# Optimization experiments

Measured on AMD Instinct MI355X. Metric: run time of the kernel, lower is better.

Reference implementation:

```python
import jax, jax.numpy as jnp
import numpy as np

NH = 8       # num attention heads (hardcoded in module)
NL = 6       # n_layers
EPS = 1e-5   # LayerNorm eps (torch default)


def pos_enc(dim, length):
    # faithful to module's positional_encoding: even cols sin, odd cols cos,
    # with angle = pos / 10000^(2i/dim) where i indexes ALL columns via arange(0,2*dim,2)/dim
    pos = jnp.arange(length, dtype=jnp.float32)[:, None]
    div = 1.0 / (10000.0 ** (jnp.arange(0, 2 * dim, 2, dtype=jnp.float32) / dim))
    ang = pos * div[None, :]  # [length, dim]
    cols = jnp.arange(dim)
    return jnp.where(cols % 2 == 0, jnp.sin(ang), jnp.cos(ang))


def layernorm(x):
    m = x.mean(-1, keepdims=True)
    v = x.var(-1, keepdims=True)  # biased, matches torch LayerNorm
    return (x - m) / jnp.sqrt(v + EPS)


def setup_inputs() -> dict:
    key = jax.random.key(0)
    ks = jax.random.split(key, 8)
    S, H = 2048, 1024
    D = H // NH
    sc = 1.0 / np.sqrt(H)  # ~ torch Linear init scale
    return {
        "inputs": jax.random.normal(ks[0], (S, H), jnp.float32),
        "Wq": jax.random.normal(ks[1], (NH, H, D), jnp.float32) * sc,
        "bq": jnp.zeros((NH, D), jnp.float32),
        "Wk": jax.random.normal(ks[2], (NH, H, D), jnp.float32) * sc,
        "bk": jnp.zeros((NH, D), jnp.float32),
        "Wv": jax.random.normal(ks[3], (NH, H, D), jnp.float32) * sc,
        "bv": jnp.zeros((NH, D), jnp.float32),
        "W1": jax.random.normal(ks[4], (H, H), jnp.float32) * sc,
        "b1": jnp.zeros((H,), jnp.float32),
        "W2": jax.random.normal(ks[5], (H, H), jnp.float32) * sc,
        "b2": jnp.zeros((H,), jnp.float32),
    }


def reference(inputs, Wq, bq, Wk, bk, Wv, bv, W1, b1, W2, b2):
    S, H = inputs.shape
    scale = jnp.sqrt(jnp.float32(H))  # module scales by sqrt(hidden), not sqrt(head_dim)
    x = inputs + pos_enc(H, S)        # [S, H]
    kv = x  # dropout in eval mode = identity; k_v_input fixed to layer-0 input (faithful)
    # K/V are identical every layer (shared weights + fixed kv input)
    K = jnp.einsum('sh,nhd->nsd', kv, Wk) + bk[:, None, :]  # [NH, S, D]
    V = jnp.einsum('sh,nhd->nsd', kv, Wv) + bv[:, None, :]
    t_in = x
    for _ in range(NL):
        Q = jnp.einsum('sh,nhd->nsd', t_in, Wq) + bq[:, None, :]
        A = jax.nn.softmax(jnp.einsum('nsd,ntd->nst', Q, K) / scale, axis=-1)
        ctx = jnp.einsum('nst,ntd->nsd', A, V)        # [NH, S, D]
        cat = ctx.transpose(1, 0, 2).reshape(S, H)    # concat heads on feature dim
        mh = layernorm(t_in + cat)
        ff = jax.nn.relu(mh @ W1 + b1) @ W2 + b2
        t_in = layernorm(mh + ff)
    return t_in
```

## Files before the change

### kernel.cpp

```cpp
#include <hip/hip_runtime.h>

#define S_LEN 2048
#define H_DIM 1024
#define NHEAD 8
#define D_HEAD 128
#define KSPLIT 2
#define KV_PER (S_LEN / KSPLIT)

typedef __bf16 bf16x8 __attribute__((ext_vector_type(8)));
typedef float floatx4 __attribute__((ext_vector_type(4)));

__device__ __forceinline__ float b2f(unsigned short u) {
    union { unsigned int i; float f; } v;
    v.i = ((unsigned int)u) << 16;
    return v.f;
}
__device__ __forceinline__ unsigned short f2b(float f) {
    union { float f; unsigned int i; } v;
    v.f = f;
    return (unsigned short)((v.i + 0x7fffu + ((v.i >> 16) & 1u)) >> 16);
}

__device__ __forceinline__ void dma16(void* lds, const void* g) {
    __builtin_amdgcn_global_load_lds(
        (const __attribute__((address_space(1))) void*)g,
        (__attribute__((address_space(3))) void*)lds, 16, 0, 0);
}

__global__ __launch_bounds__(256) void posenc_kernel(
    const float* __restrict__ in, float* __restrict__ xf,
    unsigned short* __restrict__ xb)
{
    int g = blockIdx.x * 256 + threadIdx.x;
    int s = g >> 10;
    int h = g & 1023;
    float dv = powf(10000.0f, -(float)h * (1.0f / 512.0f));
    float ang = (float)s * dv;
    float pe = (h & 1) ? cosf(ang) : sinf(ang);
    float x = in[g] + pe;
    xf[g] = x;
    xb[g] = f2b(x);
}

__global__ __launch_bounds__(256) void transpose_all(
    const float* __restrict__ Wq, const float* __restrict__ Wk,
    const float* __restrict__ Wv, const float* __restrict__ W1,
    const float* __restrict__ W2,
    unsigned short* __restrict__ WqT, unsigned short* __restrict__ WkT,
    unsigned short* __restrict__ WvT, unsigned short* __restrict__ W1T,
    unsigned short* __restrict__ W2T)
{
    __shared__ unsigned short tile[32][33];
    const int z = blockIdx.z;
    const float* ih;
    unsigned short* oh;
    int ldin;
    if (z < 8)       { ih = Wq + (size_t)z * 131072;        oh = WqT + (size_t)z * 131072;        ldin = 128; }
    else if (z < 16) { ih = Wk + (size_t)(z - 8) * 131072;  oh = WkT + (size_t)(z - 8) * 131072;  ldin = 128; }
    else if (z < 24) { ih = Wv + (size_t)(z - 16) * 131072; oh = WvT + (size_t)(z - 16) * 131072; ldin = 128; }
    else if (z < 32) { ih = W1 + (size_t)(z - 24) * 128;    oh = W1T + (size_t)(z - 24) * 131072; ldin = 1024; }
    else             { ih = W2 + (size_t)(z - 32) * 128;    oh = W2T + (size_t)(z - 32) * 131072; ldin = 1024; }
    const int r0 = blockIdx.y * 32, c0 = blockIdx.x * 32;
    const int tx = threadIdx.x, ty = threadIdx.y;
    for (int i = ty; i < 32; i += 8)
        tile[i][tx] = f2b(ih[(size_t)(r0 + i) * ldin + c0 + tx]);
    __syncthreads();
    for (int i = ty; i < 32; i += 8)
        oh[(size_t)(c0 + i) * 1024 + r0 + tx] = tile[tx][i];
}

template <int MODE, bool RELU>
__device__ __forceinline__ void gemm128_core(
    unsigned short* sA, unsigned short* sB,
    const unsigned short* A, const unsigned short* Bt,
    const float* bias, float* Cf, unsigned short* Cb, int ldt, int i0, int j0)
{
    const int K = H_DIM;
    const int tid = threadIdx.x;
    const int wave = tid >> 6, lane = tid & 63;
    const int quad = lane >> 4, l16 = lane & 15;
    const int wm = (wave >> 1) * 64, wn = (wave & 1) * 64;

    const int srow = lane >> 3;
    const int schunk = (lane & 7) ^ srow;
    const unsigned short* Ap = A + (size_t)(i0 + wave * 8 + srow) * K + schunk * 8;
    const unsigned short* Bp = Bt + (size_t)(j0 + wave * 8 + srow) * K + schunk * 8;

    floatx4 z4 = {0.f, 0.f, 0.f, 0.f};
    floatx4 acc[4][4];
#pragma unroll
    for (int i = 0; i < 4; i++)
#pragma unroll
        for (int j = 0; j < 4; j++) acc[i][j] = z4;

#pragma unroll
    for (int it = 0; it < 4; it++) {
        const int lb = (wave * 8 + it * 32) * 64;
        dma16(sA + lb, Ap + (size_t)(it * 32) * K);
        dma16(sB + lb, Bp + (size_t)(it * 32) * K);
    }
    __syncthreads();

    int buf = 0;
    for (int k0 = 0; k0 < K; k0 += 64) {
        if (k0 + 64 < K) {
            unsigned short* nA = sA + (buf ^ 1) * 8192;
            unsigned short* nB = sB + (buf ^ 1) * 8192;
#pragma unroll
            for (int it = 0; it < 4; it++) {
                const int lb = (wave * 8 + it * 32) * 64;
                dma16(nA + lb, Ap + (size_t)(it * 32) * K + k0 + 64);
                dma16(nB + lb, Bp + (size_t)(it * 32) * K + k0 + 64);
            }
        }
        const unsigned short* cA = sA + buf * 8192;
        const unsigned short* cB = sB + buf * 8192;
#pragma unroll
        for (int kh = 0; kh < 2; kh++) {
            bf16x8 af[4], bfr[4];
#pragma unroll
            for (int mi = 0; mi < 4; mi++) {
                int row = wm + mi * 16 + l16;
                int p = (kh * 4 + quad) ^ (l16 & 7);
                af[mi] = *(const bf16x8*)(cA + row * 64 + p * 8);
            }
#pragma unroll
            for (int ni = 0; ni < 4; ni++) {
                int row = wn + ni * 16 + l16;
                int p = (kh * 4 + quad) ^ (l16 & 7);
                bfr[ni] = *(const bf16x8*)(cB + row * 64 + p * 8);
            }
#pragma unroll
            for (int mi = 0; mi < 4; mi++)
#pragma unroll
                for (int ni = 0; ni < 4; ni++)
                    acc[mi][ni] = __builtin_amdgcn_mfma_f32_16x16x32_bf16(
                        af[mi], bfr[ni], acc[mi][ni], 0, 0, 0);
        }
        __syncthreads();
        buf ^= 1;
    }

#pragma unroll
    for (int mi = 0; mi < 4; mi++) {
#pragma unroll
        for (int ni = 0; ni < 4; ni++) {
            const int col = j0 + wn + ni * 16 + l16;
            const float bval = bias[col];
#pragma unroll
            for (int r = 0; r < 4; r++) {
                const int row_o = i0 + wm + mi * 16 + quad * 4 + r;
                float v = acc[mi][ni][r] + bval;
                if (RELU) v = fmaxf(v, 0.0f);
                if (MODE == 0) Cb[(size_t)row_o * H_DIM + col] = f2b(v);
                else if (MODE == 1) Cb[(size_t)col * ldt + row_o] = f2b(v);
                else Cf[(size_t)row_o * H_DIM + col] = v;
            }
        }
    }
}

template <int MODE, bool RELU>
__global__ __launch_bounds__(256, 2) void gemm128(
    const unsigned short* __restrict__ A, const unsigned short* __restrict__ Bt,
    const float* __restrict__ bias, float* __restrict__ Cf,
    unsigned short* __restrict__ Cb, int ldt)
{
    extern __shared__ __align__(16) unsigned short gsm[];
    gemm128_core<MODE, RELU>(gsm, gsm + 16384, A, Bt, bias, Cf, Cb, ldt,
                             blockIdx.y * 128, blockIdx.x * 128);
}

__global__ __launch_bounds__(256, 2) void gemm_kv(
    const unsigned short* __restrict__ A,
    const unsigned short* __restrict__ WkT, const unsigned short* __restrict__ WvT,
    const float* __restrict__ bk, const float* __restrict__ bv,
    unsigned short* __restrict__ Kb, unsigned short* __restrict__ Vtb)
{
    extern __shared__ __align__(16) unsigned short gsm[];
    if (blockIdx.z == 0)
        gemm128_core<0, false>(gsm, gsm + 16384, A, WkT, bk, nullptr, Kb, 0,
                               blockIdx.y * 128, blockIdx.x * 128);
    else
        gemm128_core<1, false>(gsm, gsm + 16384, A, WvT, bv, nullptr, Vtb, S_LEN,
                               blockIdx.y * 128, blockIdx.x * 128);
}

__global__ __launch_bounds__(256, 2) void flash_attn(
    const unsigned short* __restrict__ Qg, const unsigned short* __restrict__ Kg,
    const unsigned short* __restrict__ Vt, unsigned short* __restrict__ Op,
    float* __restrict__ Lp)
{
    extern __shared__ __align__(16) unsigned short smem[];
    unsigned short* sK0 = smem;
    unsigned short* sV0 = smem + 16384;
    unsigned short* sP = smem + 32768;

    const int tid = threadIdx.x;
    const int wave = tid >> 6, lane = tid & 63;
    const int quad = lane >> 4, l16 = lane & 15;
    const int head = blockIdx.y;
    const int q0 = blockIdx.x * 64;
    const int split = blockIdx.z;
    const int h0 = head * D_HEAD;

    bf16x8 aq[4];
    const int qrow = q0 + wave * 16 + l16;
#pragma unroll
    for (int ks = 0; ks < 4; ks++)
        aq[ks] = *(const bf16x8*)(Qg + (size_t)qrow * H_DIM + h0 + ks * 32 + quad * 8);

    unsigned short* myP = sP + wave * (16 * 72);

    const int k_r = wave * 4 + (lane >> 4);
    const int k_c = (lane & 15) ^ (k_r & 15);
    const int v_r = wave * 8 + (lane >> 3);
    const int v_c = (lane & 7) ^ (v_r & 7);

    const unsigned short* Kbase = Kg + h0;
    const unsigned short* Vbase = Vt + (size_t)h0 * S_LEN;
    const int kt0 = split * KV_PER;

    floatx4 z4 = {0.f, 0.f, 0.f, 0.f};
    floatx4 o[8];
#pragma unroll
    for (int i = 0; i < 8; i++) o[i] = z4;
    float l_r[4] = {0.f, 0.f, 0.f, 0.f};

#pragma unroll
    for (int it = 0; it < 4; it++) {
        dma16(sK0 + (wave * 4 + it * 16) * 128,
              Kbase + (size_t)(kt0 + k_r + it * 16) * H_DIM + k_c * 8);
        dma16(sV0 + (wave * 8 + it * 32) * 64,
              Vbase + (size_t)(v_r + it * 32) * S_LEN + kt0 + v_c * 8);
    }
    __syncthreads();

    int buf = 0;
    for (int it0 = 0; it0 < KV_PER; it0 += 64) {
        const int t0 = kt0 + it0;
        if (it0 + 64 < KV_PER) {
            const int nt = t0 + 64;
            unsigned short* nK = sK0 + (buf ^ 1) * 8192;
            unsigned short* nV = sV0 + (buf ^ 1) * 8192;
#pragma unroll
            for (int it = 0; it < 4; it++) {
                dma16(nK + (wave * 4 + it * 16) * 128,
                      Kbase + (size_t)(nt + k_r + it * 16) * H_DIM + k_c * 8);
                dma16(nV + (wave * 8 + it * 32) * 64,
                      Vbase + (size_t)(v_r + it * 32) * S_LEN + nt + v_c * 8);
            }
        }
        const unsigned short* cK = sK0 + buf * 8192;
        const unsigned short* cV = sV0 + buf * 8192;

        floatx4 sc[4];
#pragma unroll
        for (int ni = 0; ni < 4; ni++) {
            sc[ni] = z4;
#pragma unroll
            for (int ks = 0; ks < 4; ks++) {
                int p = (ks * 4 + quad) ^ l16;
                bf16x8 bk = *(const bf16x8*)(cK + (ni * 16 + l16) * 128 + p * 8);
                sc[ni] = __builtin_amdgcn_mfma_f32_16x16x32_bf16(aq[ks], bk, sc[ni], 0, 0, 0);
            }
        }

#pragma unroll
        for (int ni = 0; ni < 4; ni++)
#pragma unroll
            for (int r = 0; r < 4; r++) {
                float p = __expf(sc[ni][r] * 0.03125f);
                sc[ni][r] = p;
                l_r[r] += p;
            }

#pragma unroll
        for (int ni = 0; ni < 4; ni++)
#pragma unroll
            for (int r = 0; r < 4; r++) {
                int prow = quad * 4 + r;
                myP[prow * 72 + ((ni * 16 + l16) ^ ((prow & 8) << 1))] = f2b(sc[ni][r]);
            }
        bf16x8 ap[2];
#pragma unroll
        for (int ks = 0; ks < 2; ks++)
            ap[ks] = *(const bf16x8*)(myP + l16 * 72 + ((ks * 32 + quad * 8) ^ ((l16 & 8) << 1)));

#pragma unroll
        for (int ni = 0; ni < 8; ni++) {
#pragma unroll
            for (int ks = 0; ks < 2; ks++) {
                int p = (ks * 4 + quad) ^ (l16 & 7);
                bf16x8 bv = *(const bf16x8*)(cV + (ni * 16 + l16) * 64 + p * 8);
                o[ni] = __builtin_amdgcn_mfma_f32_16x16x32_bf16(ap[ks], bv, o[ni], 0, 0, 0);
            }
        }

        __syncthreads();
        buf ^= 1;
    }

#pragma unroll
    for (int r = 0; r < 4; r++)
#pragma unroll
        for (int off = 1; off < 16; off <<= 1)
            l_r[r] += __shfl_xor(l_r[r], off, 64);

#pragma unroll
    for (int r = 0; r < 4; r++) {
        float inv = 1.0f / l_r[r];
        int row = q0 + wave * 16 + quad * 4 + r;
#pragma unroll
        for (int ni = 0; ni < 8; ni++)
            Op[((size_t)split * S_LEN + row) * H_DIM + h0 + ni * 16 + l16] =
                f2b(o[ni][r] * inv);
        if (l16 == 0)
            Lp[(split * NHEAD + head) * S_LEN + row] = l_r[r];
    }
}

__global__ __launch_bounds__(256) void merge_add_layernorm(
    const float* __restrict__ t, const unsigned short* __restrict__ Op,
    const float* __restrict__ Lp,
    float* __restrict__ of, unsigned short* __restrict__ ob)
{
    __shared__ float red[8];
    const int row = blockIdx.x, tid = threadIdx.x;
    const int head = tid >> 5;
    const size_t base = (size_t)row * H_DIM + tid * 4;

    float l_s[KSPLIT];
    ushort4 os[KSPLIT];
#pragma unroll
    for (int sp = 0; sp < KSPLIT; sp++) {
        os[sp] = *(const ushort4*)(Op + ((size_t)sp * S_LEN + row) * H_DIM + tid * 4);
        l_s[sp] = Lp[(sp * NHEAD + head) * S_LEN + row];
    }
    float W = 0.f, a0 = 0.f, a1 = 0.f, a2 = 0.f, a3 = 0.f;
#pragma unroll
    for (int sp = 0; sp < KSPLIT; sp++) {
        float w = l_s[sp];
        W += w;
        a0 += w * b2f(os[sp].x);
        a1 += w * b2f(os[sp].y);
        a2 += w * b2f(os[sp].z);
        a3 += w * b2f(os[sp].w);
    }
    float inv = 1.0f / W;
    float4 x = *(const float4*)(t + base);
    float v0 = x.x + a0 * inv, v1 = x.y + a1 * inv;
    float v2 = x.z + a2 * inv, v3 = x.w + a3 * inv;

    float s = v0 + v1 + v2 + v3;
    float q = v0 * v0 + v1 * v1 + v2 * v2 + v3 * v3;
#pragma unroll
    for (int off = 32; off >= 1; off >>= 1) {
        s += __shfl_xor(s, off, 64);
        q += __shfl_xor(q, off, 64);
    }
    if ((tid & 63) == 0) { red[tid >> 6] = s; red[4 + (tid >> 6)] = q; }
    __syncthreads();
    s = red[0] + red[1] + red[2] + red[3];
    q = red[4] + red[5] + red[6] + red[7];
    const float mean = s * (1.0f / (float)H_DIM);
    const float var = q * (1.0f / (float)H_DIM) - mean * mean;
    const float rstd = rsqrtf(var + 1e-5f);
    float o0 = (v0 - mean) * rstd, o1 = (v1 - mean) * rstd;
    float o2 = (v2 - mean) * rstd, o3 = (v3 - mean) * rstd;
    *(float4*)(of + base) = make_float4(o0, o1, o2, o3);
    *(ushort4*)(ob + base) = make_ushort4(f2b(o0), f2b(o1), f2b(o2), f2b(o3));
}

__global__ __launch_bounds__(256) void add_layernorm(
    const float* __restrict__ a, const float* __restrict__ b,
    float* __restrict__ of, unsigned short* __restrict__ ob)
{
    __shared__ float red[8];
    const int row = blockIdx.x, tid = threadIdx.x;
    const size_t base = (size_t)row * H_DIM + tid * 4;
    float4 x = *(const float4*)(a + base);
    float4 y = *(const float4*)(b + base);
    float v0 = x.x + y.x, v1 = x.y + y.y, v2 = x.z + y.z, v3 = x.w + y.w;
    float s = v0 + v1 + v2 + v3;
    float q = v0 * v0 + v1 * v1 + v2 * v2 + v3 * v3;
#pragma unroll
    for (int off = 32; off >= 1; off >>= 1) {
        s += __shfl_xor(s, off, 64);
        q += __shfl_xor(q, off, 64);
    }
    if ((tid & 63) == 0) { red[tid >> 6] = s; red[4 + (tid >> 6)] = q; }
    __syncthreads();
    s = red[0] + red[1] + red[2] + red[3];
    q = red[4] + red[5] + red[6] + red[7];
    const float mean = s * (1.0f / (float)H_DIM);
    const float var = q * (1.0f / (float)H_DIM) - mean * mean;
    const float rstd = rsqrtf(var + 1e-5f);
    float o0 = (v0 - mean) * rstd, o1 = (v1 - mean) * rstd;
    float o2 = (v2 - mean) * rstd, o3 = (v3 - mean) * rstd;
    *(float4*)(of + base) = make_float4(o0, o1, o2, o3);
    *(ushort4*)(ob + base) = make_ushort4(f2b(o0), f2b(o1), f2b(o2), f2b(o3));
}

extern "C" void kernel_launch(void* const* d_in, const int* in_sizes, int n_in,
                              void* d_out, int out_size, void* d_ws, size_t ws_size,
                              hipStream_t stream)
{
    (void)in_sizes; (void)n_in; (void)out_size; (void)ws_size;
    const float* in = (const float*)d_in[0];
    const float* Wq = (const float*)d_in[1];
    const float* bq = (const float*)d_in[2];
    const float* Wk = (const float*)d_in[3];
    const float* bk = (const float*)d_in[4];
    const float* Wv = (const float*)d_in[5];
    const float* bv = (const float*)d_in[6];
    const float* W1 = (const float*)d_in[7];
    const float* b1 = (const float*)d_in[8];
    const float* W2 = (const float*)d_in[9];
    const float* b2 = (const float*)d_in[10];

    char* ws = (char*)d_ws;
    const size_t MB = 1024 * 1024;
    float* t_f32 = (float*)(ws + 0 * MB);
    float* cf_f32 = (float*)(ws + 8 * MB);
    unsigned short* t_b = (unsigned short*)(ws + 16 * MB);
    unsigned short* K_b = (unsigned short*)(ws + 20 * MB);
    unsigned short* Vt_b = (unsigned short*)(ws + 24 * MB);
    unsigned short* Q_b = (unsigned short*)(ws + 28 * MB);
    unsigned short* WqT = (unsigned short*)(ws + 32 * MB);
    unsigned short* WkT = (unsigned short*)(ws + 34 * MB);
    unsigned short* WvT = (unsigned short*)(ws + 36 * MB);
    unsigned short* W1T = (unsigned short*)(ws + 38 * MB);
    unsigned short* W2T = (unsigned short*)(ws + 40 * MB);
    unsigned short* Op = (unsigned short*)(ws + 42 * MB);
    float* Lp = (float*)(ws + 58 * MB);

    (void)hipFuncSetAttribute(reinterpret_cast<const void*>(&flash_attn),
                              hipFuncAttributeMaxDynamicSharedMemorySize, 74752);
    (void)hipFuncSetAttribute(reinterpret_cast<const void*>(&gemm128<0, false>),
                              hipFuncAttributeMaxDynamicSharedMemorySize, 65536);
    (void)hipFuncSetAttribute(reinterpret_cast<const void*>(&gemm128<0, true>),
                              hipFuncAttributeMaxDynamicSharedMemorySize, 65536);
    (void)hipFuncSetAttribute(reinterpret_cast<const void*>(&gemm128<2, false>),
                              hipFuncAttributeMaxDynamicSharedMemorySize, 65536);
    (void)hipFuncSetAttribute(reinterpret_cast<const void*>(&gemm_kv),
                              hipFuncAttributeMaxDynamicSharedMemorySize, 65536);

    transpose_all<<<dim3(4, 32, 40), dim3(32, 8), 0, stream>>>(
        Wq, Wk, Wv, W1, W2, WqT, WkT, WvT, W1T, W2T);

    posenc_kernel<<<(S_LEN * H_DIM) / 256, 256, 0, stream>>>(in, t_f32, t_b);

    dim3 gg(H_DIM / 128, S_LEN / 128);
    gemm_kv<<<dim3(8, 16, 2), 256, 65536, stream>>>(t_b, WkT, WvT, bk, bv, K_b, Vt_b);

    for (int layer = 0; layer < 6; layer++) {
        gemm128<0, false><<<gg, 256, 65536, stream>>>(t_b, WqT, bq, nullptr, Q_b, 0);
        flash_attn<<<dim3(S_LEN / 64, NHEAD, KSPLIT), 256, 74752, stream>>>(Q_b, K_b, Vt_b, Op, Lp);
        merge_add_layernorm<<<S_LEN, 256, 0, stream>>>(t_f32, Op, Lp, t_f32, t_b);
        gemm128<0, true><<<gg, 256, 65536, stream>>>(t_b, W1T, b1, nullptr, Q_b, 0);
        gemm128<2, false><<<gg, 256, 65536, stream>>>(Q_b, W2T, b2, cf_f32, nullptr, 0);
        float* of = (layer == 5) ? (float*)d_out : t_f32;
        add_layernorm<<<S_LEN, 256, 0, stream>>>(t_f32, cf_f32, of, t_b);
    }
}
```

Measured before the change: 593.9 us.

## Fuse split-KV merge and residual layernorms into GEMM A-operand staging

Removes the separate merge_add_layernorm and per-layer add_layernorm kernels. Each GEMM block now computes row statistics for its 128 rows and normalizes the residual sum on the fly while staging the bf16 A tile. Blocks with j0==0 also write the fp32 normalized rows needed for the next residual. This saves launches and intermediate round trips, but each of the 8 column blocks recomputes the row statistics and the A-tile loads become synchronous register work. A separate change remaps block indices so that blocks sharing rows land on the same XCD for L2 reuse.

New measurement: 2.335 ms. 3.93x slower.

```diff
diff --git a/kernel.cpp b/kernel.cpp
--- a/kernel.cpp
+++ b/kernel.cpp
@@ -9,6 +9,7 @@
 
 typedef __bf16 bf16x8 __attribute__((ext_vector_type(8)));
 typedef float floatx4 __attribute__((ext_vector_type(4)));
+typedef unsigned short ushortx8 __attribute__((ext_vector_type(8)));
 
 __device__ __forceinline__ float b2f(unsigned short u) {
     union { unsigned int i; float f; } v;
@@ -25,6 +26,13 @@
     __builtin_amdgcn_global_load_lds(
         (const __attribute__((address_space(1))) void*)g,
         (__attribute__((address_space(3))) void*)lds, 16, 0, 0);
+}
+
+__device__ __forceinline__ void xcd_map(int& i0, int& j0) {
+    int id = blockIdx.x + (blockIdx.y << 3);
+    int xcd = id & 7, slot = id >> 3;
+    i0 = (xcd + ((slot >> 3) << 3)) * 128;
+    j0 = (slot & 7) * 128;
 }
 
 __global__ __launch_bounds__(256) void posenc_kernel(
@@ -69,22 +77,168 @@
         oh[(size_t)(c0 + i) * 1024 + r0 + tx] = tile[tx][i];
 }
 
-template <int MODE, bool RELU>
-__device__ __forceinline__ void gemm128_core(
-    unsigned short* sA, unsigned short* sB,
-    const unsigned short* A, const unsigned short* Bt,
-    const float* bias, float* Cf, unsigned short* Cb, int ldt, int i0, int j0)
-{
-    const int K = H_DIM;
+template <int FUSE>
+__device__ __forceinline__ void stageA_f(
+    unsigned short* dstA, int kn, int i0,
+    const float* in1, const float* in2,
+    const unsigned short* OpP, const float* sW,
+    const float* my_m, const float* my_r, int wave, int lane)
+{
+    const int srow = lane >> 3;
+    const int schunk = (lane & 7) ^ srow;
+    const int h = kn >> 7;
+#pragma unroll
+    for (int it = 0; it < 4; it++) {
+        const int rl = wave * 8 + srow + it * 32;
+        const size_t gb = (size_t)(i0 + rl) * H_DIM + kn + schunk * 8;
+        float v[8];
+        float4 a0 = *(const float4*)(in1 + gb);
+        float4 a1 = *(const float4*)(in1 + gb + 4);
+        if (FUSE == 1) {
+            float4 b0 = *(const float4*)(in2 + gb);
+            float4 b1 = *(const float4*)(in2 + gb + 4);
+            v[0] = a0.x + b0.x; v[1] = a0.y + b0.y; v[2] = a0.z + b0.z; v[3] = a0.w + b0.w;
+            v[4] = a1.x + b1.x; v[5] = a1.y + b1.y; v[6] = a1.z + b1.z; v[7] = a1.w + b1.w;
+        } else {
+            const unsigned short* o0 = OpP + gb;
+            const unsigned short* o1 = o0 + (size_t)S_LEN * H_DIM;
+            ushort4 u0 = *(const ushort4*)o0, u1 = *(const ushort4*)(o0 + 4);
+            ushort4 t0 = *(const ushort4*)o1, t1 = *(const ushort4*)(o1 + 4);
+            float w0 = sW[(rl * 8 + h) * 2], w1 = sW[(rl * 8 + h) * 2 + 1];
+            v[0] = a0.x + w0 * b2f(u0.x) + w1 * b2f(t0.x);
+            v[1] = a0.y + w0 * b2f(u0.y) + w1 * b2f(t0.y);
+            v[2] = a0.z + w0 * b2f(u0.z) + w1 * b2f(t0.z);
+            v[3] = a0.w + w0 * b2f(u0.w) + w1 * b2f(t0.w);
+            v[4] = a1.x + w0 * b2f(u1.x) + w1 * b2f(t1.x);
+            v[5] = a1.y + w0 * b2f(u1.y) + w1 * b2f(t1.y);
+            v[6] = a1.z + w0 * b2f(u1.z) + w1 * b2f(t1.z);
+            v[7] = a1.w + w0 * b2f(u1.w) + w1 * b2f(t1.w);
+        }
+        const float m = my_m[it], rs = my_r[it];
+        ushortx8 pk;
+#pragma unroll
+        for (int e = 0; e < 8; e++) pk[e] = f2b((v[e] - m) * rs);
+        *(ushortx8*)(dstA + rl * 64 + (lane & 7) * 8) = pk;
+    }
+}
+
+template <int MODE, bool RELU, int FUSE>
+__device__ __forceinline__ void gemm_core(
+    unsigned short* sA, unsigned short* sB, float* sStat, float* sW,
+    const unsigned short* Abf, const unsigned short* Bt, const float* bias,
+    float* Cf, unsigned short* Cb, int ldt,
+    const float* in1, const float* in2,
+    const unsigned short* OpP, const float* LpP, float* xout,
+    int i0, int j0)
+{
     const int tid = threadIdx.x;
     const int wave = tid >> 6, lane = tid & 63;
     const int quad = lane >> 4, l16 = lane & 15;
     const int wm = (wave >> 1) * 64, wn = (wave & 1) * 64;
-
     const int srow = lane >> 3;
     const int schunk = (lane & 7) ^ srow;
-    const unsigned short* Ap = A + (size_t)(i0 + wave * 8 + srow) * K + schunk * 8;
-    const unsigned short* Bp = Bt + (size_t)(j0 + wave * 8 + srow) * K + schunk * 8;
+
+    float my_m[4], my_r[4];
+
+    if (FUSE) {
+        if (FUSE == 2) {
+            for (int e = tid; e < 1024; e += 256) {
+                int r = e >> 3, h = e & 7;
+                float l0 = LpP[h * S_LEN + i0 + r];
+                float l1 = LpP[(NHEAD + h) * S_LEN + i0 + r];
+                float inv = 1.f / (l0 + l1);
+                sW[e * 2] = l0 * inv; sW[e * 2 + 1] = l1 * inv;
+            }
+            __syncthreads();
+        }
+        {
+            const int r = tid >> 1, hf = tid & 1;
+            const float* p1 = in1 + (size_t)(i0 + r) * H_DIM + hf * 512;
+            float s = 0.f, q = 0.f;
+            if (FUSE == 1) {
+                const float* p2 = in2 + (size_t)(i0 + r) * H_DIM + hf * 512;
+                for (int c = 0; c < 512; c += 4) {
+                    float4 a = *(const float4*)(p1 + c);
+                    float4 b = *(const float4*)(p2 + c);
+                    float v0 = a.x + b.x, v1 = a.y + b.y, v2 = a.z + b.z, v3 = a.w + b.w;
+                    s += v0 + v1 + v2 + v3;
+                    q += v0 * v0 + v1 * v1 + v2 * v2 + v3 * v3;
+                }
+            } else {
+                const unsigned short* o0 = OpP + (size_t)(i0 + r) * H_DIM + hf * 512;
+                const unsigned short* o1 = o0 + (size_t)S_LEN * H_DIM;
+                for (int h4 = 0; h4 < 4; h4++) {
+                    int h = hf * 4 + h4;
+                    float w0 = sW[(r * 8 + h) * 2], w1 = sW[(r * 8 + h) * 2 + 1];
+                    for (int c = h4 * 128; c < h4 * 128 + 128; c += 4) {
+                        float4 a = *(const float4*)(p1 + c);
+                        ushort4 u = *(const ushort4*)(o0 + c);
+                        ushort4 t = *(const ushort4*)(o1 + c);
+                        float v0 = a.x + w0 * b2f(u.x) + w1 * b2f(t.x);
+                        float v1 = a.y + w0 * b2f(u.y) + w1 * b2f(t.y);
+                        float v2 = a.z + w0 * b2f(u.z) + w1 * b2f(t.z);
+                        float v3 = a.w + w0 * b2f(u.w) + w1 * b2f(t.w);
+                        s += v0 + v1 + v2 + v3;
+                        q += v0 * v0 + v1 * v1 + v2 * v2 + v3 * v3;
+                    }
+                }
+            }
+            s += __shfl_xor(s, 1, 64);
+            q += __shfl_xor(q, 1, 64);
+            if (hf == 0) {
+                float mean = s * (1.f / 1024.f);
+                float var = q * (1.f / 1024.f) - mean * mean;
+                sStat[r * 2] = mean;
+                sStat[r * 2 + 1] = rsqrtf(var + 1e-5f);
+            }
+        }
+        __syncthreads();
+        if (xout != nullptr && j0 == 0) {
+            const int r = tid >> 1, hf = tid & 1;
+            const float mean = sStat[r * 2], rstd = sStat[r * 2 + 1];
+            float* po = xout + (size_t)(i0 + r) * H_DIM + hf * 512;
+            const float* p1 = in1 + (size_t)(i0 + r) * H_DIM + hf * 512;
+            if (FUSE == 1) {
+                const float* p2 = in2 + (size_t)(i0 + r) * H_DIM + hf * 512;
+                for (int c = 0; c < 512; c += 4) {
+                    float4 a = *(const float4*)(p1 + c);
+                    float4 b = *(const float4*)(p2 + c);
+                    float4 o;
+                    o.x = (a.x + b.x - mean) * rstd; o.y = (a.y + b.y - mean) * rstd;
+                    o.z = (a.z + b.z - mean) * rstd; o.w = (a.w + b.w - mean) * rstd;
+                    *(float4*)(po + c) = o;
+                }
+            } else {
+                const unsigned short* o0 = OpP + (size_t)(i0 + r) * H_DIM + hf * 512;
+                const unsigned short* o1 = o0 + (size_t)S_LEN * H_DIM;
+                for (int h4 = 0; h4 < 4; h4++) {
+                    int h = hf * 4 + h4;
+                    float w0 = sW[(r * 8 + h) * 2], w1 = sW[(r * 8 + h) * 2 + 1];
+                    for (int c = h4 * 128; c < h4 * 128 + 128; c += 4) {
+                        float4 a = *(const float4*)(p1 + c);
+                        ushort4 u = *(const ushort4*)(o0 + c);
+                        ushort4 t = *(const ushort4*)(o1 + c);
+                        float4 o;
+                        o.x = (a.x + w0 * b2f(u.x) + w1 * b2f(t.x) - mean) * rstd;
+                        o.y = (a.y + w0 * b2f(u.y) + w1 * b2f(t.y) - mean) * rstd;
+                        o.z = (a.z + w0 * b2f(u.z) + w1 * b2f(t.z) - mean) * rstd;
+                        o.w = (a.w + w0 * b2f(u.w) + w1 * b2f(t.w) - mean) * rstd;
+                        *(float4*)(po + c) = o;
+                    }
+                }
+            }
+        }
+#pragma unroll
+        for (int it = 0; it < 4; it++) {
+            int rl = wave * 8 + srow + it * 32;
+            my_m[it] = sStat[rl * 2];
+            my_r[it] = sStat[rl * 2 + 1];
+        }
+    }
+
+    const unsigned short* Ap = (FUSE == 0)
+        ? Abf + (size_t)(i0 + wave * 8 + srow) * H_DIM + schunk * 8 : nullptr;
+    const unsigned short* Bp = Bt + (size_t)(j0 + wave * 8 + srow) * H_DIM + schunk * 8;
 
     floatx4 z4 = {0.f, 0.f, 0.f, 0.f};
     floatx4 acc[4][4];
@@ -93,24 +247,34 @@
 #pragma unroll
         for (int j = 0; j < 4; j++) acc[i][j] = z4;
 
-#pragma unroll
-    for (int it = 0; it < 4; it++) {
-        const int lb = (wave * 8 + it * 32) * 64;
-        dma16(sA + lb, Ap + (size_t)(it * 32) * K);
-        dma16(sB + lb, Bp + (size_t)(it * 32) * K);
-    }
+    if (FUSE == 0) {
+#pragma unroll
+        for (int it = 0; it < 4; it++)
+            dma16(sA + (wave * 8 + it * 32) * 64, Ap + (size_t)(it * 32) * H_DIM);
+    } else {
+        stageA_f<FUSE>(sA, 0, i0, in1, in2, OpP, sW, my_m, my_r, wave, lane);
+    }
+#pragma unroll
+    for (int it = 0; it < 4; it++)
+        dma16(sB + (wave * 8 + it * 32) * 64, Bp + (size_t)(it * 32) * H_DIM);
     __syncthreads();
 
     int buf = 0;
-    for (int k0 = 0; k0 < K; k0 += 64) {
-        if (k0 + 64 < K) {
+    for (int k0 = 0; k0 < H_DIM; k0 += 64) {
+        if (k0 + 64 < H_DIM) {
             unsigned short* nA = sA + (buf ^ 1) * 8192;
             unsigned short* nB = sB + (buf ^ 1) * 8192;
 #pragma unroll
-            for (int it = 0; it < 4; it++) {
-                const int lb = (wave * 8 + it * 32) * 64;
-                dma16(nA + lb, Ap + (size_t)(it * 32) * K + k0 + 64);
-                dma16(nB + lb, Bp + (size_t)(it * 32) * K + k0 + 64);
+            for (int it = 0; it < 4; it++)
+                dma16(nB + (wave * 8 + it * 32) * 64,
+                      Bp + (size_t)(it * 32) * H_DIM + k0 + 64);
+            if (FUSE == 0) {
+#pragma unroll
+                for (int it = 0; it < 4; it++)
+                    dma16(nA + (wave * 8 + it * 32) * 64,
+                          Ap + (size_t)(it * 32) * H_DIM + k0 + 64);
+            } else {
+                stageA_f<FUSE>(nA, k0 + 64, i0, in1, in2, OpP, sW, my_m, my_r, wave, lane);
             }
         }
         const unsigned short* cA = sA + buf * 8192;
@@ -161,14 +325,42 @@
 }
 
 template <int MODE, bool RELU>
-__global__ __launch_bounds__(256, 2) void gemm128(
+__global__ __launch_bounds__(256, 2) void gemm_plain(
     const unsigned short* __restrict__ A, const unsigned short* __restrict__ Bt,
     const float* __restrict__ bias, float* __restrict__ Cf,
-    unsigned short* __restrict__ Cb, int ldt)
+    unsigned short* __restrict__ Cb)
 {
     extern __shared__ __align__(16) unsigned short gsm[];
-    gemm128_core<MODE, RELU>(gsm, gsm + 16384, A, Bt, bias, Cf, Cb, ldt,
-                             blockIdx.y * 128, blockIdx.x * 128);
+    int i0, j0; xcd_map(i0, j0);
+    gemm_core<MODE, RELU, 0>(gsm, gsm + 16384, nullptr, nullptr, A, Bt, bias,
+                             Cf, Cb, 0, nullptr, nullptr, nullptr, nullptr, nullptr,
+                             i0, j0);
+}
+
+__global__ __launch_bounds__(256, 2) void gemm_fuse_add(
+    const float* __restrict__ in1, const float* __restrict__ in2,
+    const unsigned short* __restrict__ Bt, const float* __restrict__ bias,
+    unsigned short* __restrict__ Cb, float* __restrict__ xout)
+{
+    extern __shared__ __align__(16) unsigned short gsm[];
+    int i0, j0; xcd_map(i0, j0);
+    gemm_core<0, false, 1>(gsm, gsm + 16384, (float*)(gsm + 32768), nullptr,
+                           nullptr, Bt, bias, nullptr, Cb, 0,
+                           in1, in2, nullptr, nullptr, xout, i0, j0);
+}
+
+__global__ __launch_bounds__(256, 2) void gemm_fuse_merge(
+    const float* __restrict__ x, const unsigned short* __restrict__ OpP,
+    const float* __restrict__ LpP,
+    const unsigned short* __restrict__ Bt, const float* __restrict__ bias,
+    unsigned short* __restrict__ Cb, float* __restrict__ mhout)
+{
+    extern __shared__ __align__(16) unsigned short gsm[];
+    int i0, j0; xcd_map(i0, j0);
+    float* sStat = (float*)(gsm + 32768);
+    gemm_core<0, true, 2>(gsm, gsm + 16384, sStat, sStat + 256,
+                          nullptr, Bt, bias, nullptr, Cb, 0,
+                          x, nullptr, OpP, LpP, mhout, i0, j0);
 }
 
 __global__ __launch_bounds__(256, 2) void gemm_kv(
@@ -178,12 +370,15 @@
     unsigned short* __restrict__ Kb, unsigned short* __restrict__ Vtb)
 {
     extern __shared__ __align__(16) unsigned short gsm[];
+    int i0, j0; xcd_map(i0, j0);
     if (blockIdx.z == 0)
-        gemm128_core<0, false>(gsm, gsm + 16384, A, WkT, bk, nullptr, Kb, 0,
-                               blockIdx.y * 128, blockIdx.x * 128);
+        gemm_core<0, false, 0>(gsm, gsm + 16384, nullptr, nullptr, A, WkT, bk,
+                               nullptr, Kb, 0, nullptr, nullptr, nullptr, nullptr,
+                               nullptr, i0, j0);
     else
-        gemm128_core<1, false>(gsm, gsm + 16384, A, WvT, bv, nullptr, Vtb, S_LEN,
-                               blockIdx.y * 128, blockIdx.x * 128);
+        gemm_core<1, false, 0>(gsm, gsm + 16384, nullptr, nullptr, A, WvT, bv,
+                               nullptr, Vtb, S_LEN, nullptr, nullptr, nullptr,
+                               nullptr, nullptr, i0, j0);
 }
 
 __global__ __launch_bounds__(256, 2) void flash_attn(
@@ -320,61 +515,9 @@
     }
 }
 
-__global__ __launch_bounds__(256) void merge_add_layernorm(
-    const float* __restrict__ t, const unsigned short* __restrict__ Op,
-    const float* __restrict__ Lp,
-    float* __restrict__ of, unsigned short* __restrict__ ob)
-{
-    __shared__ float red[8];
-    const int row = blockIdx.x, tid = threadIdx.x;
-    const int head = tid >> 5;
-    const size_t base = (size_t)row * H_DIM + tid * 4;
-
-    float l_s[KSPLIT];
-    ushort4 os[KSPLIT];
-#pragma unroll
-    for (int sp = 0; sp < KSPLIT; sp++) {
-        os[sp] = *(const ushort4*)(Op + ((size_t)sp * S_LEN + row) * H_DIM + tid * 4);
-        l_s[sp] = Lp[(sp * NHEAD + head) * S_LEN + row];
-    }
-    float W = 0.f, a0 = 0.f, a1 = 0.f, a2 = 0.f, a3 = 0.f;
-#pragma unroll
-    for (int sp = 0; sp < KSPLIT; sp++) {
-        float w = l_s[sp];
-        W += w;
-        a0 += w * b2f(os[sp].x);
-        a1 += w * b2f(os[sp].y);
-        a2 += w * b2f(os[sp].z);
-        a3 += w * b2f(os[sp].w);
-    }
-    float inv = 1.0f / W;
-    float4 x = *(const float4*)(t + base);
-    float v0 = x.x + a0 * inv, v1 = x.y + a1 * inv;
-    float v2 = x.z + a2 * inv, v3 = x.w + a3 * inv;
-
-    float s = v0 + v1 + v2 + v3;
-    float q = v0 * v0 + v1 * v1 + v2 * v2 + v3 * v3;
-#pragma unroll
-    for (int off = 32; off >= 1; off >>= 1) {
-        s += __shfl_xor(s, off, 64);
-        q += __shfl_xor(q, off, 64);
-    }
-    if ((tid & 63) == 0) { red[tid >> 6] = s; red[4 + (tid >> 6)] = q; }
-    __syncthreads();
-    s = red[0] + red[1] + red[2] + red[3];
-    q = red[4] + red[5] + red[6] + red[7];
-    const float mean = s * (1.0f / (float)H_DIM);
-    const float var = q * (1.0f / (float)H_DIM) - mean * mean;
-    const float rstd = rsqrtf(var + 1e-5f);
-    float o0 = (v0 - mean) * rstd, o1 = (v1 - mean) * rstd;
-    float o2 = (v2 - mean) * rstd, o3 = (v3 - mean) * rstd;
-    *(float4*)(of + base) = make_float4(o0, o1, o2, o3);
-    *(ushort4*)(ob + base) = make_ushort4(f2b(o0), f2b(o1), f2b(o2), f2b(o3));
-}
-
 __global__ __launch_bounds__(256) void add_layernorm(
     const float* __restrict__ a, const float* __restrict__ b,
-    float* __restrict__ of, unsigned short* __restrict__ ob)
+    float* __restrict__ of)
 {
     __shared__ float red[8];
     const int row = blockIdx.x, tid = threadIdx.x;
@@ -396,10 +539,8 @@
     const float mean = s * (1.0f / (float)H_DIM);
     const float var = q * (1.0f / (float)H_DIM) - mean * mean;
     const float rstd = rsqrtf(var + 1e-5f);
-    float o0 = (v0 - mean) * rstd, o1 = (v1 - mean) * rstd;
-    float o2 = (v2 - mean) * rstd, o3 = (v3 - mean) * rstd;
-    *(float4*)(of + base) = make_float4(o0, o1, o2, o3);
-    *(ushort4*)(ob + base) = make_ushort4(f2b(o0), f2b(o1), f2b(o2), f2b(o3));
+    *(float4*)(of + base) = make_float4((v0 - mean) * rstd, (v1 - mean) * rstd,
+                                        (v2 - mean) * rstd, (v3 - mean) * rstd);
 }
 
 extern "C" void kernel_launch(void* const* d_in, const int* in_sizes, int n_in,
@@ -421,46 +562,56 @@
 
     char* ws = (char*)d_ws;
     const size_t MB = 1024 * 1024;
-    float* t_f32 = (float*)(ws + 0 * MB);
-    float* cf_f32 = (float*)(ws + 8 * MB);
-    unsigned short* t_b = (unsigned short*)(ws + 16 * MB);
-    unsigned short* K_b = (unsigned short*)(ws + 20 * MB);
-    unsigned short* Vt_b = (unsigned short*)(ws + 24 * MB);
-    unsigned short* Q_b = (unsigned short*)(ws + 28 * MB);
-    unsigned short* WqT = (unsigned short*)(ws + 32 * MB);
-    unsigned short* WkT = (unsigned short*)(ws + 34 * MB);
-    unsigned short* WvT = (unsigned short*)(ws + 36 * MB);
-    unsigned short* W1T = (unsigned short*)(ws + 38 * MB);
-    unsigned short* W2T = (unsigned short*)(ws + 40 * MB);
-    unsigned short* Op = (unsigned short*)(ws + 42 * MB);
-    float* Lp = (float*)(ws + 58 * MB);
+    float* x0_f32 = (float*)(ws + 0 * MB);
+    float* mh_f32 = (float*)(ws + 8 * MB);
+    float* cf_f32 = (float*)(ws + 16 * MB);
+    float* xb_f32 = (float*)(ws + 24 * MB);
+    unsigned short* t_b = (unsigned short*)(ws + 32 * MB);
+    unsigned short* K_b = (unsigned short*)(ws + 36 * MB);
+    unsigned short* Vt_b = (unsigned short*)(ws + 40 * MB);
+    unsigned short* Q_b = (unsigned short*)(ws + 44 * MB);
+    unsigned short* WqT = (unsigned short*)(ws + 48 * MB);
+    unsigned short* WkT = (unsigned short*)(ws + 50 * MB);
+    unsigned short* WvT = (unsigned short*)(ws + 52 * MB);
+    unsigned short* W1T = (unsigned short*)(ws + 54 * MB);
+    unsigned short* W2T = (unsigned short*)(ws + 56 * MB);
+    unsigned short* Op = (unsigned short*)(ws + 58 * MB);
+    float* Lp = (float*)(ws + 66 * MB);
 
     (void)hipFuncSetAttribute(reinterpret_cast<const void*>(&flash_attn),
                               hipFuncAttributeMaxDynamicSharedMemorySize, 74752);
-    (void)hipFuncSetAttribute(reinterpret_cast<const void*>(&gemm128<0, false>),
+    (void)hipFuncSetAttribute(reinterpret_cast<const void*>(&gemm_plain<0, false>),
                               hipFuncAttributeMaxDynamicSharedMemorySize, 65536);
-    (void)hipFuncSetAttribute(reinterpret_cast<const void*>(&gemm128<0, true>),
+    (void)hipFuncSetAttribute(reinterpret_cast<const void*>(&gemm_plain<2, false>),
                               hipFuncAttributeMaxDynamicSharedMemorySize, 65536);
-    (void)hipFuncSetAttribute(reinterpret_cast<const void*>(&gemm128<2, false>),
-                              hipFuncAttributeMaxDynamicSharedMemorySize, 65536);
+    (void)hipFuncSetAttribute(reinterpret_cast<const void*>(&gemm_fuse_add),
+                              hipFuncAttributeMaxDynamicSharedMemorySize, 66560);
+    (void)hipFuncSetAttribute(reinterpret_cast<const void*>(&gemm_fuse_merge),
+                              hipFuncAttributeMaxDynamicSharedMemorySize, 74752);
     (void)hipFuncSetAttribute(reinterpret_cast<const void*>(&gemm_kv),
                               hipFuncAttributeMaxDynamicSharedMemorySize, 65536);
 
     transpose_all<<<dim3(4, 32, 40), dim3(32, 8), 0, stream>>>(
         Wq, Wk, Wv, W1, W2, WqT, WkT, WvT, W1T, W2T);
 
-    posenc_kernel<<<(S_LEN * H_DIM) / 256, 256, 0, stream>>>(in, t_f32, t_b);
-
-    dim3 gg(H_DIM / 128, S_LEN / 128);
+    posenc_kernel<<<(S_LEN * H_DIM) / 256, 256, 0, stream>>>(in, x0_f32, t_b);
+
     gemm_kv<<<dim3(8, 16, 2), 256, 65536, stream>>>(t_b, WkT, WvT, bk, bv, K_b, Vt_b);
 
+    dim3 gg(8, 16);
     for (int layer = 0; layer < 6; layer++) {
-        gemm128<0, false><<<gg, 256, 65536, stream>>>(t_b, WqT, bq, nullptr, Q_b, 0);
-        flash_attn<<<dim3(S_LEN / 64, NHEAD, KSPLIT), 256, 74752, stream>>>(Q_b, K_b, Vt_b, Op, Lp);
-        merge_add_layernorm<<<S_LEN, 256, 0, stream>>>(t_f32, Op, Lp, t_f32, t_b);
-        gemm128<0, true><<<gg, 256, 65536, stream>>>(t_b, W1T, b1, nullptr, Q_b, 0);
-        gemm128<2, false><<<gg, 256, 65536, stream>>>(Q_b, W2T, b2, cf_f32, nullptr, 0);
-        float* of = (layer == 5) ? (float*)d_out : t_f32;
-        add_layernorm<<<S_LEN, 256, 0, stream>>>(t_f32, cf_f32, of, t_b);
-    }
-}
+        const float* xA;
+        if (layer == 0) {
+            gemm_plain<0, false><<<gg, 256, 65536, stream>>>(t_b, WqT, bq, nullptr, Q_b);
+            xA = x0_f32;
+        } else {
+            gemm_fuse_add<<<gg, 256, 66560, stream>>>(mh_f32, cf_f32, WqT, bq, Q_b, xb_f32);
+            xA = xb_f32;
+        }
+        flash_attn<<<dim3(S_LEN / 64, NHEAD, KSPLIT), 256, 74752, stream>>>(
+            Q_b, K_b, Vt_b, Op, Lp);
+        gemm_fuse_merge<<<gg, 256, 74752, stream>>>(xA, Op, Lp, W1T, b1, Q_b, mh_f32);
+        gemm_plain<2, false><<<gg, 256, 65536, stream>>>(Q_b, W2T, b2, cf_f32, nullptr);
+    }
+    add_layernorm<<<S_LEN, 256, 0, stream>>>(mh_f32, cf_f32, (float*)d_out);
+}
```
